# Performance work log

Measured on AMD Instinct MI355X. Metric: run time of the kernel, lower is better.

Reference implementation:

```python
import jax, jax.numpy as jnp
import numpy as np

NUM_HEADS = 16
HEAD_DIM = 128
QUERY_DIM = 2048
SCALE = HEAD_DIM ** -0.5


def setup_inputs() -> dict:
    key = jax.random.key(0)
    ks = jax.random.split(key, 11)
    B, L, D = 2, 2048, QUERY_DIM
    HD = NUM_HEADS * HEAD_DIM
    s = 0.02
    return {
        "x_q": jax.random.normal(ks[0], (B, L, D), jnp.float32),
        "x_k": jax.random.normal(ks[1], (B, L, D), jnp.float32),
        "x_v": jax.random.normal(ks[2], (B, L, D), jnp.float32),
        "Wq": jax.random.normal(ks[3], (D, HD), jnp.float32) * s,
        "bq": jnp.zeros((HD,), jnp.float32),
        "Wk": jax.random.normal(ks[4], (D, HD), jnp.float32) * s,
        "bk": jnp.zeros((HD,), jnp.float32),
        "Wv": jax.random.normal(ks[5], (D, HD), jnp.float32) * s,
        "bv": jnp.zeros((HD,), jnp.float32),
        "Wo": jax.random.normal(ks[6], (HD, D), jnp.float32) * s,
        "bo": jnp.zeros((D,), jnp.float32),
    }


def _split_heads(x):  # [b, l, h*d] -> [b, h, l, d]
    b, l, _ = x.shape
    return x.reshape(b, l, NUM_HEADS, HEAD_DIM).transpose(0, 2, 1, 3)


def reference(x_q, x_k, x_v, Wq, bq, Wk, bk, Wv, bv, Wo, bo):
    # Note: the torch module constructs norm_q/norm_k but NEVER applies them in forward.
    q = _split_heads(x_q @ Wq + bq)  # [b, h, l, d]
    k = _split_heads(x_k @ Wk + bk)
    v = _split_heads(x_v @ Wv + bv)
    scores = jnp.einsum("bhid,bhjd->bhij", q, k) * SCALE
    probs = jax.nn.softmax(scores, axis=-1)
    o = jnp.einsum("bhij,bhjd->bhid", probs, v)  # [b, h, l, d]
    b, h, l, d = o.shape
    o = o.transpose(0, 2, 1, 3).reshape(b, l, h * d)
    return o @ Wo + bo
```

## Files before the change

### kernel.cpp

```cpp
#include <hip/hip_runtime.h>


typedef _Float16 f16;
typedef __attribute__((ext_vector_type(8))) _Float16 f16x8;
typedef __attribute__((ext_vector_type(4))) _Float16 f16x4;
typedef __attribute__((ext_vector_type(4))) float f32x4;
typedef __attribute__((ext_vector_type(4))) unsigned int u32x4;

#define QSCALE (0.08838834764831845f * 1.4426950408889634f)
#define SWZ3(r) (((r) & 3) | (((r) >> 1) & 4))
#define SWZV(r) ((r) & 7)

static __device__ __forceinline__ void gload16(void* lds, const void* g) {
  __builtin_amdgcn_global_load_lds(
      (__attribute__((address_space(1))) void*)g,
      (__attribute__((address_space(3))) void*)lds, 16, 0, 0);
}

__global__ __launch_bounds__(256) void cvt_x_kernel(
    const float* __restrict__ x0, const float* __restrict__ x1,
    const float* __restrict__ x2, f16* __restrict__ out) {
  const float* x = blockIdx.z == 0 ? x0 : (blockIdx.z == 1 ? x1 : x2);
  f16* o = out + (size_t)blockIdx.z * 8388608;
  size_t i = ((size_t)blockIdx.x * 256 + threadIdx.x) * 8;
  f32x4 a = *(const f32x4*)(x + i);
  f32x4 b = *(const f32x4*)(x + i + 4);
  f16x8 r;
  r[0] = (f16)a[0]; r[1] = (f16)a[1]; r[2] = (f16)a[2]; r[3] = (f16)a[3];
  r[4] = (f16)b[0]; r[5] = (f16)b[1]; r[6] = (f16)b[2]; r[7] = (f16)b[3];
  *(f16x8*)(o + i) = r;
}

__global__ __launch_bounds__(256) void cvt_w_kernel(
    const float* __restrict__ w0, const float* __restrict__ w1,
    const float* __restrict__ w2, const float* __restrict__ w3,
    f16* __restrict__ out) {
  const float* W = blockIdx.z == 0 ? w0 : blockIdx.z == 1 ? w1
                 : blockIdx.z == 2 ? w2 : w3;
  f16* WT = out + (size_t)blockIdx.z * 4194304;
  __shared__ f16 tile[64][68];
  const int tx = threadIdx.x & 15, ty = threadIdx.x >> 4;
  const int k0 = blockIdx.y * 64, n0 = blockIdx.x * 64;
#pragma unroll
  for (int i = 0; i < 4; ++i) {
    int r = ty + i * 16;
    f32x4 v = *(const f32x4*)(W + (size_t)(k0 + r) * 2048 + n0 + tx * 4);
    tile[r][tx * 4 + 0] = (f16)v[0]; tile[r][tx * 4 + 1] = (f16)v[1];
    tile[r][tx * 4 + 2] = (f16)v[2]; tile[r][tx * 4 + 3] = (f16)v[3];
  }
  __syncthreads();
#pragma unroll
  for (int i = 0; i < 4; ++i) {
    int n = ty + i * 16;
    f16x4 o;
    o[0] = tile[tx * 4 + 0][n]; o[1] = tile[tx * 4 + 1][n];
    o[2] = tile[tx * 4 + 2][n]; o[3] = tile[tx * 4 + 3][n];
    *(f16x4*)(WT + (size_t)(n0 + n) * 2048 + k0 + tx * 4) = o;
  }
}

template <int MODE>
__global__ __launch_bounds__(512, 2) void gemm128_kernel(
    const f16* __restrict__ Abase, const f16* __restrict__ Btbase,
    void* __restrict__ Obase, const float* __restrict__ b0,
    const float* __restrict__ b1, const float* __restrict__ b2) {
  const int lid = blockIdx.x;
  int bn, bm, z;
  if (MODE == 0) {
    const int logi = (lid & 7) * 96 + (lid >> 3);
    bn = logi & 7; bm = (logi >> 3) & 31; z = logi >> 8;
  } else {
    const int logi = (lid & 7) * 32 + (lid >> 3);
    bn = logi & 7; bm = logi >> 3; z = 0;
  }
  const f16* A  = Abase  + (size_t)z * 8388608;
  const f16* Bt = Btbase + (size_t)z * 4194304;
  const float* bias = z == 0 ? b0 : (z == 1 ? b1 : b2);
  const float qsc = (MODE == 0 && z == 0) ? QSCALE : 1.0f;
  const int tid = threadIdx.x, lane = tid & 63, w = tid >> 6;
  const int wm = w >> 2, wn = w & 3;
  const int l15 = lane & 15, lg = lane >> 4;
  __shared__ alignas(16) char smb[98304];

  f32x4 acc[4][4];
#pragma unroll
  for (int i = 0; i < 4; ++i)
#pragma unroll
    for (int j = 0; j < 4; ++j) acc[i][j] = (f32x4)0.f;

#define GSTAGE(KT, C_)                                                        \
  {                                                                           \
    char* Ab_ = smb + (C_) * 49152;                                           \
    char* Bb_ = Ab_ + 16384;                                                  \
    _Pragma("unroll") for (int p = 0; p < 2; ++p) {                           \
      int L = p * 8192 + tid * 16;                                            \
      int row = L >> 7, pcol = L & 127;                                       \
      int scol = pcol ^ ((row & 7) << 4);                                     \
      gload16(Ab_ + L,                                                        \
              (const char*)A + ((size_t)(bm * 128 + row) * 2048 + (KT) * 64) * 2 + scol); \
    }                                                                         \
    _Pragma("unroll") for (int p = 0; p < 4; ++p) {                           \
      int L = p * 8192 + tid * 16;                                            \
      int row = L >> 7, pcol = L & 127;                                       \
      int scol = pcol ^ ((row & 7) << 4);                                     \
      gload16(Bb_ + L,                                                        \
              (const char*)Bt + ((size_t)(bn * 256 + row) * 2048 + (KT) * 64) * 2 + scol); \
    }                                                                         \
  }

#define GREADS(H)                                                             \
  _Pragma("unroll") for (int i = 0; i < 4; ++i) {                             \
    int row = wm * 64 + i * 16 + l15;                                         \
    af[H][i] = *(const f16x8*)(Ab + row * 128 +                               \
                               (((H) * 64 + lg * 16) ^ ((row & 7) << 4)));    \
  }                                                                           \
  _Pragma("unroll") for (int j = 0; j < 4; ++j) {                             \
    int row = wn * 64 + j * 16 + l15;                                         \
    bf[H][j] = *(const f16x8*)(Bb + row * 128 +                               \
                               (((H) * 64 + lg * 16) ^ ((row & 7) << 4)));    \
  }

#define GMFMA(H)                                                              \
  __builtin_amdgcn_s_setprio(1);                                              \
  _Pragma("unroll") for (int i = 0; i < 4; ++i)                               \
    _Pragma("unroll") for (int j = 0; j < 4; ++j)                             \
      acc[i][j] = __builtin_amdgcn_mfma_f32_16x16x32_f16(                     \
          af[H][i], bf[H][j], acc[i][j], 0, 0, 0);                            \
  __builtin_amdgcn_s_setprio(0);

  GSTAGE(0, 0);
#pragma unroll 1
  for (int kt = 0; kt < 32; ++kt) {
    const int c = kt & 1;
    if (kt < 31) {
      GSTAGE(kt + 1, c ^ 1);
      asm volatile("s_waitcnt vmcnt(6)" ::: "memory");
    } else {
      asm volatile("s_waitcnt vmcnt(0)" ::: "memory");
    }
    __builtin_amdgcn_s_barrier();

    const char* Ab = smb + c * 49152;
    const char* Bb = Ab + 16384;
    f16x8 af[2][4], bf[2][4];
    GREADS(0);
    asm volatile("s_waitcnt lgkmcnt(0)" ::: "memory");
    __builtin_amdgcn_sched_barrier(0);
    GMFMA(0);
    GREADS(1);
    __builtin_amdgcn_sched_barrier(0);
    __builtin_amdgcn_s_barrier();
    asm volatile("s_waitcnt lgkmcnt(0)" ::: "memory");
    __builtin_amdgcn_sched_barrier(0);
    GMFMA(1);
  }

  if (MODE == 0) {
    f16* Oz = (f16*)Obase + (size_t)z * 8388608;
#pragma unroll
    for (int i = 0; i < 4; ++i)
#pragma unroll
      for (int j = 0; j < 4; ++j) {
        int col = bn * 256 + wn * 64 + j * 16 + l15;
        int h = col >> 7, d = col & 127;
        float bv = bias[col];
#pragma unroll
        for (int r = 0; r < 4; ++r) {
          int rowg = bm * 128 + wm * 64 + i * 16 + lg * 4 + r;
          int b_ = rowg >> 11, lpos = rowg & 2047;
          Oz[(size_t)(b_ * 16 + h) * 262144 + (size_t)lpos * 128 + d] =
              (f16)((acc[i][j][r] + bv) * qsc);
        }
      }
  } else {
    float* Out = (float*)Obase;
#pragma unroll
    for (int i = 0; i < 4; ++i)
#pragma unroll
      for (int j = 0; j < 4; ++j) {
        int col = bn * 256 + wn * 64 + j * 16 + l15;
        float bv = bias[col];
#pragma unroll
        for (int r = 0; r < 4; ++r) {
          int rowg = bm * 128 + wm * 64 + i * 16 + lg * 4 + r;
          Out[(size_t)rowg * 2048 + col] = acc[i][j][r] + bv;
        }
      }
  }
#undef GSTAGE
#undef GREADS
#undef GMFMA
}

__global__ __launch_bounds__(256) void tr_v_kernel(const f16* __restrict__ v,
                                                   f16* __restrict__ vtout) {
  const int bh = blockIdx.z;
  const f16* V = v + (size_t)bh * 262144;
  f16* VT = vtout + (size_t)bh * 262144;
  __shared__ f16 tile[64][68];
  const int tx = threadIdx.x & 15, ty = threadIdx.x >> 4;
  const int l0 = blockIdx.x * 64, d0 = blockIdx.y * 64;
#pragma unroll
  for (int i = 0; i < 4; ++i) {
    int r = ty + i * 16;
    f16x4 val = *(const f16x4*)(V + (size_t)(l0 + r) * 128 + d0 + tx * 4);
    tile[r][tx * 4 + 0] = val[0]; tile[r][tx * 4 + 1] = val[1];
    tile[r][tx * 4 + 2] = val[2]; tile[r][tx * 4 + 3] = val[3];
  }
  __syncthreads();
#pragma unroll
  for (int i = 0; i < 4; ++i) {
    int d = ty + i * 16;
    f16x4 o;
    o[0] = tile[tx * 4 + 0][d]; o[1] = tile[tx * 4 + 1][d];
    o[2] = tile[tx * 4 + 2][d]; o[3] = tile[tx * 4 + 3][d];
    *(f16x4*)(VT + (size_t)(d0 + d) * 2048 + l0 + tx * 4) = o;
  }
}

__global__ __launch_bounds__(512, 4) void attn_kernel(
    const f16* __restrict__ q, const f16* __restrict__ k,
    const f16* __restrict__ vt, f16* __restrict__ o) {
  const int orig = blockIdx.y * 16 + blockIdx.x;
  const int swz = (orig & 7) * 64 + (orig >> 3);
  const int qt = swz & 15, bh = swz >> 4;
  const int tid = threadIdx.x, lane = tid & 63, w = tid >> 6;
  const int l15 = lane & 15, lg = lane >> 4;
  const f16* Qb = q + (size_t)bh * 262144 + (size_t)qt * 128 * 128;
  const char* Kb = (const char*)(k + (size_t)bh * 262144);
  const char* Vtb = (const char*)(vt + (size_t)bh * 262144);
  __shared__ alignas(16) char sm[65536];

  f16x8 qf[4];
#pragma unroll
  for (int ks = 0; ks < 4; ++ks)
    qf[ks] = *(const f16x8*)(Qb + (w * 16 + l15) * 128 + ks * 32 + lg * 8);

  f32x4 oacc[8];
#pragma unroll
  for (int df = 0; df < 8; ++df) oacc[df] = (f32x4)0.f;
  float mrow = -1e30f, ps = 0.f;
  const int rA = ((l15 >> 2) << 3) + (l15 & 3);

#define STAGE(T, B)                                                          \
  {                                                                          \
    char* Ks_ = sm + (B) * 32768;                                            \
    char* Vs_ = Ks_ + 16384;                                                 \
    _Pragma("unroll") for (int i = 0; i < 2; ++i) {                          \
      int c = i * 8 + w;                                                     \
      int phys = c * 1024 + lane * 16;                                       \
      {                                                                      \
        int row = phys >> 8, pcol = phys & 255;                              \
        int lcol = pcol ^ (SWZ3(row) << 4);                                  \
        gload16(Ks_ + c * 1024, Kb + (size_t)((T) * 64 + row) * 256 + lcol); \
      }                                                                      \
      {                                                                      \
        int row = phys >> 7, pcol = phys & 127;                              \
        int lcol = pcol ^ (SWZV(row) << 4);                                  \
        gload16(Vs_ + c * 1024, Vtb + (size_t)row * 4096 + (T) * 128 + lcol);\
      }                                                                      \
    }                                                                        \
  }

  STAGE(0, 0);
  int cur = 0;
  for (int t = 0; t < 32; ++t) {
    __syncthreads();
    if (t < 31) STAGE(t + 1, cur ^ 1);
    const char* Ks = sm + cur * 32768;
    const char* Vs = Ks + 16384;

    f32x4 s[4];
#pragma unroll
    for (int nf = 0; nf < 4; ++nf) s[nf] = (f32x4)0.f;
    __builtin_amdgcn_s_setprio(1);
#pragma unroll
    for (int ks = 0; ks < 4; ++ks) {
      f16x8 kf[4];
#pragma unroll
      for (int nf = 0; nf < 4; ++nf) {
        int row = ((nf & 1) << 5) + ((nf >> 1) << 2) + rA;
        int colb = (ks * 64 + lg * 16) ^ (SWZ3(row) << 4);
        kf[nf] = *(const f16x8*)(Ks + row * 256 + colb);
      }
#pragma unroll
      for (int nf = 0; nf < 4; ++nf)
        s[nf] = __builtin_amdgcn_mfma_f32_16x16x32_f16(kf[nf], qf[ks], s[nf], 0, 0, 0);
    }
    __builtin_amdgcn_s_setprio(0);

    unsigned int pk[2][4];
    {
      float m0 = fmaxf(fmaxf(s[0][0], s[0][1]), fmaxf(s[0][2], s[0][3]));
      float m1 = fmaxf(fmaxf(s[1][0], s[1][1]), fmaxf(s[1][2], s[1][3]));
      float m2 = fmaxf(fmaxf(s[2][0], s[2][1]), fmaxf(s[2][2], s[2][3]));
      float m3 = fmaxf(fmaxf(s[3][0], s[3][1]), fmaxf(s[3][2], s[3][3]));
      float mx = fmaxf(fmaxf(m0, m1), fmaxf(m2, m3));
      mx = fmaxf(mx, __shfl_xor(mx, 16));
      mx = fmaxf(mx, __shfl_xor(mx, 32));
      if (!__all(mx <= mrow + 8.f)) {
        float mnew = fmaxf(mrow, mx);
        float sc = exp2f(mrow - mnew);
        mrow = mnew;
        ps *= sc;
#pragma unroll
        for (int r = 0; r < 4; ++r) {
          float scr = __shfl(sc, (lane & 48) | (lg * 4 + r));
#pragma unroll
          for (int df = 0; df < 8; ++df) oacc[df][r] *= scr;
        }
      }
      float m = mrow;
      float psum = 0.f;
#pragma unroll
      for (int nf = 0; nf < 4; ++nf)
#pragma unroll
        for (int h = 0; h < 2; ++h) {
          float p0 = exp2f(s[nf][2 * h] - m);
          float p1 = exp2f(s[nf][2 * h + 1] - m);
          psum += p0 + p1;
          pk[nf & 1][(nf >> 1) * 2 + h] =
              __builtin_bit_cast(unsigned int, __builtin_amdgcn_cvt_pkrtz(p0, p1));
        }
      ps += psum;
    }

    __builtin_amdgcn_s_setprio(1);
#pragma unroll
    for (int kvs = 0; kvs < 2; ++kvs) {
      f16x8 pa = __builtin_bit_cast(f16x8, *(const u32x4*)pk[kvs]);
#pragma unroll
      for (int df = 0; df < 8; ++df) {
        int row = df * 16 + l15;
        int colb = (kvs * 64 + lg * 16) ^ (SWZV(row) << 4);
        f16x8 vb = *(const f16x8*)(Vs + row * 128 + colb);
        oacc[df] = __builtin_amdgcn_mfma_f32_16x16x32_f16(pa, vb, oacc[df], 0, 0, 0);
      }
    }
    __builtin_amdgcn_s_setprio(0);
    cur ^= 1;
  }

  const int b_ = bh >> 4, h_ = bh & 15;
  f16* Ob = o + (size_t)b_ * 4194304 + (size_t)qt * 128 * 2048 + h_ * 128;
  float lr = ps;
  lr += __shfl_xor(lr, 16);
  lr += __shfl_xor(lr, 32);
  float inv = 1.f / lr;
#pragma unroll
  for (int r = 0; r < 4; ++r) {
    float invr = __shfl(inv, (lane & 48) | (lg * 4 + r));
    int rl = w * 16 + lg * 4 + r;
#pragma unroll
    for (int df = 0; df < 8; ++df)
      Ob[(size_t)rl * 2048 + df * 16 + l15] = (f16)(oacc[df][r] * invr);
  }
#undef STAGE
}

extern "C" void kernel_launch(void* const* d_in, const int* in_sizes, int n_in,
                              void* d_out, int out_size, void* d_ws, size_t ws_size,
                              hipStream_t stream) {
  const float* xq = (const float*)d_in[0];
  const float* xk = (const float*)d_in[1];
  const float* xv = (const float*)d_in[2];
  const float* Wq = (const float*)d_in[3];
  const float* bq = (const float*)d_in[4];
  const float* Wk = (const float*)d_in[5];
  const float* bk = (const float*)d_in[6];
  const float* Wv = (const float*)d_in[7];
  const float* bv = (const float*)d_in[8];
  const float* Wo = (const float*)d_in[9];
  const float* bo = (const float*)d_in[10];

  char* ws = (char*)d_ws;
  f16* xh   = (f16*)(ws);
  f16* wt   = (f16*)(ws + 50331648);
  f16* qkv  = (f16*)(ws + 83886080);
  f16* vtb  = (f16*)(ws);
  f16* oatt = (f16*)(ws + 16777216);
  float* outp = (float*)d_out;

  hipLaunchKernelGGL(cvt_x_kernel, dim3(4096, 1, 3), dim3(256), 0, stream,
                     xq, xk, xv, xh);
  hipLaunchKernelGGL(cvt_w_kernel, dim3(32, 32, 4), dim3(256), 0, stream,
                     Wq, Wk, Wv, Wo, wt);
  hipLaunchKernelGGL((gemm128_kernel<0>), dim3(768), dim3(512), 0, stream,
                     xh, wt, (void*)qkv, bq, bk, bv);
  hipLaunchKernelGGL(tr_v_kernel, dim3(32, 2, 32), dim3(256), 0, stream,
                     qkv + (size_t)2 * 8388608, vtb);
  hipLaunchKernelGGL(attn_kernel, dim3(16, 32), dim3(512), 0, stream,
                     qkv, qkv + (size_t)8388608, vtb, oatt);
  hipLaunchKernelGGL((gemm128_kernel<1>), dim3(256), dim3(512), 0, stream,
                     oatt, wt + (size_t)3 * 4194304, (void*)outp, bo, bo, bo);
}
```

Before: 291.9 us.

## Shrink GEMM K-step to 32 and narrow output GEMM tile for occupancy

The K tile in both GEMMs drops from 64 to 32, which halves the LDS staging buffers, and the swizzle changes to match the shorter rows. Launch bounds now request 4 blocks per CU instead of 2. The output projection GEMM uses a 128-wide N tile and launches 512 blocks instead of 256 so more CUs have work. The cost is twice as many K iterations, each with its own barriers, and less MFMA work between syncs.

```diff
diff --git a/kernel.cpp b/kernel.cpp
--- a/kernel.cpp
+++ b/kernel.cpp
@@ -10,6 +10,7 @@
 #define QSCALE (0.08838834764831845f * 1.4426950408889634f)
 #define SWZ3(r) (((r) & 3) | (((r) >> 1) & 4))
 #define SWZV(r) ((r) & 7)
+#define SWZG(r) (((r) >> 1) & 3)
 
 static __device__ __forceinline__ void gload16(void* lds, const void* g) {
   __builtin_amdgcn_global_load_lds(
@@ -60,18 +61,23 @@
 }
 
 template <int MODE>
-__global__ __launch_bounds__(512, 2) void gemm128_kernel(
+__global__ __launch_bounds__(512, 4) void gemm128_kernel(
     const f16* __restrict__ Abase, const f16* __restrict__ Btbase,
     void* __restrict__ Obase, const float* __restrict__ b0,
     const float* __restrict__ b1, const float* __restrict__ b2) {
+  constexpr int BN = MODE == 0 ? 256 : 128;
+  constexpr int NJ = MODE == 0 ? 4 : 2;
+  constexpr int NSPAN = MODE == 0 ? 64 : 32;
+  constexpr int BLOADS = MODE == 0 ? 2 : 1;
+  constexpr int BUFSZ = 8192 + BN * 64;
   const int lid = blockIdx.x;
   int bn, bm, z;
   if (MODE == 0) {
     const int logi = (lid & 7) * 96 + (lid >> 3);
     bn = logi & 7; bm = (logi >> 3) & 31; z = logi >> 8;
   } else {
-    const int logi = (lid & 7) * 32 + (lid >> 3);
-    bn = logi & 7; bm = logi >> 3; z = 0;
+    const int logi = (lid & 7) * 64 + (lid >> 3);
+    bn = logi & 15; bm = logi >> 4; z = 0;
   }
   const f16* A  = Abase  + (size_t)z * 8388608;
   const f16* Bt = Btbase + (size_t)z * 4194304;
@@ -80,79 +86,73 @@
   const int tid = threadIdx.x, lane = tid & 63, w = tid >> 6;
   const int wm = w >> 2, wn = w & 3;
   const int l15 = lane & 15, lg = lane >> 4;
-  __shared__ alignas(16) char smb[98304];
-
-  f32x4 acc[4][4];
+  __shared__ alignas(16) char smb[2 * BUFSZ];
+
+  f32x4 acc[4][NJ];
 #pragma unroll
   for (int i = 0; i < 4; ++i)
 #pragma unroll
-    for (int j = 0; j < 4; ++j) acc[i][j] = (f32x4)0.f;
+    for (int j = 0; j < NJ; ++j) acc[i][j] = (f32x4)0.f;
 
 #define GSTAGE(KT, C_)                                                        \
   {                                                                           \
-    char* Ab_ = smb + (C_) * 49152;                                           \
-    char* Bb_ = Ab_ + 16384;                                                  \
-    _Pragma("unroll") for (int p = 0; p < 2; ++p) {                           \
+    char* Ab_ = smb + (C_) * BUFSZ;                                           \
+    char* Bb_ = Ab_ + 8192;                                                   \
+    {                                                                         \
+      int L = tid * 16;                                                       \
+      int row = L >> 6, pcol = L & 63;                                        \
+      int scol = pcol ^ (SWZG(row) << 4);                                     \
+      gload16(Ab_ + L,                                                        \
+              (const char*)A + ((size_t)(bm * 128 + row) * 2048 + (KT) * 32) * 2 + scol); \
+    }                                                                         \
+    _Pragma("unroll") for (int p = 0; p < BLOADS; ++p) {                      \
       int L = p * 8192 + tid * 16;                                            \
-      int row = L >> 7, pcol = L & 127;                                       \
-      int scol = pcol ^ ((row & 7) << 4);                                     \
-      gload16(Ab_ + L,                                                        \
-              (const char*)A + ((size_t)(bm * 128 + row) * 2048 + (KT) * 64) * 2 + scol); \
+      int row = L >> 6, pcol = L & 63;                                        \
+      int scol = pcol ^ (SWZG(row) << 4);                                     \
+      gload16(Bb_ + L,                                                        \
+              (const char*)Bt + ((size_t)(bn * BN + row) * 2048 + (KT) * 32) * 2 + scol); \
     }                                                                         \
-    _Pragma("unroll") for (int p = 0; p < 4; ++p) {                           \
-      int L = p * 8192 + tid * 16;                                            \
-      int row = L >> 7, pcol = L & 127;                                       \
-      int scol = pcol ^ ((row & 7) << 4);                                     \
-      gload16(Bb_ + L,                                                        \
-              (const char*)Bt + ((size_t)(bn * 256 + row) * 2048 + (KT) * 64) * 2 + scol); \
-    }                                                                         \
-  }
-
-#define GREADS(H)                                                             \
-  _Pragma("unroll") for (int i = 0; i < 4; ++i) {                             \
-    int row = wm * 64 + i * 16 + l15;                                         \
-    af[H][i] = *(const f16x8*)(Ab + row * 128 +                               \
-                               (((H) * 64 + lg * 16) ^ ((row & 7) << 4)));    \
-  }                                                                           \
-  _Pragma("unroll") for (int j = 0; j < 4; ++j) {                             \
-    int row = wn * 64 + j * 16 + l15;                                         \
-    bf[H][j] = *(const f16x8*)(Bb + row * 128 +                               \
-                               (((H) * 64 + lg * 16) ^ ((row & 7) << 4)));    \
-  }
-
-#define GMFMA(H)                                                              \
-  __builtin_amdgcn_s_setprio(1);                                              \
-  _Pragma("unroll") for (int i = 0; i < 4; ++i)                               \
-    _Pragma("unroll") for (int j = 0; j < 4; ++j)                             \
-      acc[i][j] = __builtin_amdgcn_mfma_f32_16x16x32_f16(                     \
-          af[H][i], bf[H][j], acc[i][j], 0, 0, 0);                            \
-  __builtin_amdgcn_s_setprio(0);
+  }
 
   GSTAGE(0, 0);
 #pragma unroll 1
-  for (int kt = 0; kt < 32; ++kt) {
+  for (int kt = 0; kt < 64; ++kt) {
     const int c = kt & 1;
-    if (kt < 31) {
+    if (kt < 63) {
       GSTAGE(kt + 1, c ^ 1);
-      asm volatile("s_waitcnt vmcnt(6)" ::: "memory");
+      if constexpr (MODE == 0)
+        asm volatile("s_waitcnt vmcnt(3)" ::: "memory");
+      else
+        asm volatile("s_waitcnt vmcnt(2)" ::: "memory");
     } else {
       asm volatile("s_waitcnt vmcnt(0)" ::: "memory");
     }
     __builtin_amdgcn_s_barrier();
 
-    const char* Ab = smb + c * 49152;
-    const char* Bb = Ab + 16384;
-    f16x8 af[2][4], bf[2][4];
-    GREADS(0);
+    const char* Ab = smb + c * BUFSZ;
+    const char* Bb = Ab + 8192;
+    f16x8 af[4], bf[NJ];
+#pragma unroll
+    for (int i = 0; i < 4; ++i) {
+      int row = wm * 64 + i * 16 + l15;
+      af[i] = *(const f16x8*)(Ab + row * 64 + ((lg * 16) ^ (SWZG(row) << 4)));
+    }
+#pragma unroll
+    for (int j = 0; j < NJ; ++j) {
+      int row = wn * NSPAN + j * 16 + l15;
+      bf[j] = *(const f16x8*)(Bb + row * 64 + ((lg * 16) ^ (SWZG(row) << 4)));
+    }
     asm volatile("s_waitcnt lgkmcnt(0)" ::: "memory");
     __builtin_amdgcn_sched_barrier(0);
-    GMFMA(0);
-    GREADS(1);
+    __builtin_amdgcn_s_setprio(1);
+#pragma unroll
+    for (int i = 0; i < 4; ++i)
+#pragma unroll
+      for (int j = 0; j < NJ; ++j)
+        acc[i][j] = __builtin_amdgcn_mfma_f32_16x16x32_f16(af[i], bf[j], acc[i][j], 0, 0, 0);
+    __builtin_amdgcn_s_setprio(0);
     __builtin_amdgcn_sched_barrier(0);
     __builtin_amdgcn_s_barrier();
-    asm volatile("s_waitcnt lgkmcnt(0)" ::: "memory");
-    __builtin_amdgcn_sched_barrier(0);
-    GMFMA(1);
   }
 
   if (MODE == 0) {
@@ -160,8 +160,8 @@
 #pragma unroll
     for (int i = 0; i < 4; ++i)
 #pragma unroll
-      for (int j = 0; j < 4; ++j) {
-        int col = bn * 256 + wn * 64 + j * 16 + l15;
+      for (int j = 0; j < NJ; ++j) {
+        int col = bn * BN + wn * NSPAN + j * 16 + l15;
         int h = col >> 7, d = col & 127;
         float bv = bias[col];
 #pragma unroll
@@ -177,8 +177,8 @@
 #pragma unroll
     for (int i = 0; i < 4; ++i)
 #pragma unroll
-      for (int j = 0; j < 4; ++j) {
-        int col = bn * 256 + wn * 64 + j * 16 + l15;
+      for (int j = 0; j < NJ; ++j) {
+        int col = bn * BN + wn * NSPAN + j * 16 + l15;
         float bv = bias[col];
 #pragma unroll
         for (int r = 0; r < 4; ++r) {
@@ -188,8 +188,6 @@
       }
   }
 #undef GSTAGE
-#undef GREADS
-#undef GMFMA
 }
 
 __global__ __launch_bounds__(256) void tr_v_kernel(const f16* __restrict__ v,
@@ -391,6 +389,6 @@
                      qkv + (size_t)2 * 8388608, vtb);
   hipLaunchKernelGGL(attn_kernel, dim3(16, 32), dim3(512), 0, stream,
                      qkv, qkv + (size_t)8388608, vtb, oatt);
-  hipLaunchKernelGGL((gemm128_kernel<1>), dim3(256), dim3(512), 0, stream,
+  hipLaunchKernelGGL((gemm128_kernel<1>), dim3(512), dim3(512), 0, stream,
                      oatt, wt + (size_t)3 * 4194304, (void*)outp, bo, bo, bo);
 }
```

Measured after the change: 296.8 us. No clear change (+1.7%).
